# Kernel optimization log

Measured on AMD Instinct MI355X. Metric: run time of the kernel, lower is better.

## Reference

```python
import jax, jax.numpy as jnp
import numpy as np

B, N = 16, 512            # graphs, atoms per graph
F_DIM, H, D = 128, 64, 16  # feature_dim, hidden_dim, far_source_dim
CUT, GROWTH = 5.0, 2.0
NS, NT = 3, 2
MULT = GROWTH ** NS        # default far_max_radius_multiplier = 8
EMAX = CUT * MULT          # 40.0
TOT = NS + NT              # 5 shells total
SF = D + 3                 # 19 per-shell features
SE_IN = TOT * SF           # 95
EH_IN = 4 * D + SE_IN      # 159
N_RBF = 8
BOUNDS = [(5.0, 10.0), (10.0, 20.0), (20.0, 40.0), (40.0, 80.0), (80.0, float('inf'))]


def ln(x, g, b):
    m = x.mean(-1, keepdims=True)
    v = x.var(-1, keepdims=True)
    return (x - m) / jnp.sqrt(v + 1e-5) * g + b


def setup_inputs() -> dict:
    key = jax.random.key(0)
    ks = jax.random.split(key, 16)
    W = lambda k, i, o: jax.random.normal(k, (i, o), jnp.float32) / np.sqrt(i)
    inp = {}
    inp['x'] = jax.random.normal(ks[0], (B * N, F_DIM), jnp.float32)
    inp['pos'] = jax.random.uniform(ks[1], (B * N, 3), jnp.float32) * 80.0
    inp['batch'] = jnp.repeat(jnp.arange(B, dtype=jnp.int32), N)
    inp['num_graphs'] = B
    inp['in_ln_g'] = jnp.ones(F_DIM); inp['in_ln_b'] = jnp.zeros(F_DIM)
    inp['src_w1'] = W(ks[2], F_DIM, H); inp['src_b1'] = jnp.zeros(H)
    inp['src_w2'] = W(ks[3], H, D);     inp['src_b2'] = jnp.zeros(D)
    inp['src_ln_g'] = jnp.ones(D); inp['src_ln_b'] = jnp.zeros(D)
    inp['se_ln_g'] = jnp.ones(SE_IN); inp['se_ln_b'] = jnp.zeros(SE_IN)
    inp['se_w1'] = W(ks[4], SE_IN, H); inp['se_b1'] = jnp.zeros(H)
    inp['se_w2'] = W(ks[5], H, D);     inp['se_b2'] = jnp.zeros(D)
    inp['eh_ln_g'] = jnp.ones(EH_IN); inp['eh_ln_b'] = jnp.zeros(EH_IN)
    inp['eh_w1'] = W(ks[6], EH_IN, H); inp['eh_b1'] = jnp.zeros(H)
    inp['eh_w2'] = W(ks[7], H, 1);     inp['eh_b2'] = jnp.zeros(1)
    inp['k_screen'] = jnp.float32(-8.0)
    inp['kg_w1'] = W(ks[8], N_RBF + 2, 32); inp['kg_b1'] = jnp.zeros(32)
    inp['kg_w2'] = jnp.zeros((32, 1)); inp['kg_b2'] = jnp.zeros(1)  # zero-init per source
    inp['far_gate'] = jnp.float32(0.2)
    inp['energy_scale'] = jnp.float32(0.0)
    return inp


def reference(x, pos, batch, num_graphs, in_ln_g, in_ln_b, src_w1, src_b1, src_w2, src_b2,
              src_ln_g, src_ln_b, se_ln_g, se_ln_b, se_w1, se_b1, se_w2, se_b2,
              eh_ln_g, eh_ln_b, eh_w1, eh_b1, eh_w2, eh_b2,
              k_screen, kg_w1, kg_b1, kg_w2, kg_b2, far_gate, energy_scale):
    M = x.shape[0]
    n = M // num_graphs
    # per-atom source features
    h = ln(x, in_ln_g, in_ln_b)
    src = jax.nn.silu(h @ src_w1 + src_b1) @ src_w2 + src_b2
    src = ln(src, src_ln_g, src_ln_b)
    # graph-wise neutralization (subtract per-graph mean)
    gsum = jax.ops.segment_sum(src, batch, num_segments=num_graphs)
    cnt = jax.ops.segment_sum(jnp.ones((M, 1), x.dtype), batch, num_segments=num_graphs)
    src = src - (gsum / jnp.maximum(cnt, 1.0))[batch]
    # pairwise distances per graph
    p = pos.reshape(num_graphs, n, 3)
    s = src.reshape(num_graphs, n, D)
    diff = p[:, :, None, :] - p[:, None, :, :]
    d = jnp.sqrt((diff * diff).sum(-1) + 1e-12)  # [B,n,n]
    not_self = ~jnp.eye(n, dtype=bool)[None]
    # physical kernel with learned RBF gate
    screening = jax.nn.softplus(k_screen)
    base = jnp.exp(-screening * d) / jnp.maximum(d, 1e-6)
    centers = jnp.linspace(CUT, EMAX, N_RBF)
    spacing = (EMAX - CUT) / (N_RBF - 1)
    gamma = 1.0 / (spacing * spacing)
    dc = d[..., None]
    rbf = jnp.exp(-gamma * (dc - centers) ** 2)
    gin = jnp.concatenate([dc / CUT, dc / EMAX, rbf], -1)
    gate = 1.0 + jnp.tanh(jax.nn.silu(gin @ kg_w1 + kg_b1) @ kg_w2 + kg_b2)[..., 0]
    ker = base * gate
    # shell statistics: kernel-weighted mean source, count, mean_r, rms_r per shell
    feats = []
    for lo, up in BOUNDS:
        m = (d >= lo) & not_self
        if np.isfinite(up):
            m = m & (d < up)
        mf = m.astype(x.dtype)
        c = mf.sum(-1)
        denom = jnp.maximum(c, 1.0)
        mean = jnp.einsum('bij,bjc->bic', ker * mf, s) / denom[..., None]
        mr = (mf * d).sum(-1) / denom
        rr = jnp.sqrt((mf * d * d).sum(-1) / denom + 1e-12)
        feats.append(jnp.concatenate([mean, c[..., None], mr[..., None], rr[..., None]], -1))
    shell = jnp.concatenate(feats, -1).reshape(M, SE_IN)  # [M, 95]
    emb = jax.nn.silu(ln(shell, se_ln_g, se_ln_b) @ se_w1 + se_b1) @ se_w2 + se_b2
    ein = jnp.concatenate([src, emb, src * emb, src - emb, shell], -1)  # [M, 159]
    pa = (jax.nn.silu(ln(ein, eh_ln_g, eh_ln_b) @ eh_w1 + eh_b1) @ eh_w2 + eh_b2)[..., 0]
    pa = pa * jnp.tanh(far_gate) * jnp.exp(energy_scale)
    return jax.ops.segment_sum(pa, batch, num_segments=num_graphs)  # per-graph energies [B]
```

## Files before the change

### kernel.cpp

```cpp
#include <hip/hip_runtime.h>
#include <hip/hip_bf16.h>
#include <math.h>

#define B_G   16
#define N_A   512
#define M_AT  8192
#define FD    128
#define HD    64
#define DD    16
#define SEIN  95
#define EHIN  159
#define NLUT  512
#define DMAXF 140.0f

__device__ __forceinline__ float silu_f(float z) { return z / (1.f + __expf(-z)); }

__global__ __launch_bounds__(128) void k_front(
    const float* __restrict__ x,
    const float* __restrict__ g, const float* __restrict__ bb,
    const float* __restrict__ w1, const float* __restrict__ b1,
    const float* __restrict__ w2, const float* __restrict__ b2,
    const float* __restrict__ lng, const float* __restrict__ lnb,
    const float* __restrict__ k_screen,
    const float* __restrict__ kg_w1, const float* __restrict__ kg_b1,
    const float* __restrict__ kg_w2, const float* __restrict__ kg_b2,
    float* __restrict__ srcout, float* __restrict__ partials,
    float2* __restrict__ lut, float* __restrict__ out) {
  int t = threadIdx.x;

  if (blockIdx.x >= 256) {
    int lb = blockIdx.x - 256;
    __shared__ float w1l[320], b1l[32], w2l[32];
    if (lb == 0 && t < B_G) out[t] = 0.f;
    for (int idx = t; idx < 320; idx += 128) w1l[idx] = kg_w1[idx];
    if (t < 32) { b1l[t] = kg_b1[t]; w2l[t] = kg_w2[t]; }
    __syncthreads();
    int i = lb * 128 + t;
    float step = DMAXF / (float)(NLUT - 1);
    float ksv = k_screen[0];
    float screening = fmaxf(ksv, 0.f) + log1pf(expf(-fabsf(ksv)));
    float b2v = kg_b2[0];
    float vals[2];
#pragma unroll
    for (int e = 0; e < 2; ++e) {
      int ii = min(i + e, NLUT - 1);
      float d = (float)ii * step;
      float base = expf(-screening * d) / fmaxf(d, 1e-6f);
      float gin[10];
      gin[0] = d * (1.f / 5.0f);
      gin[1] = d * (1.f / 40.0f);
#pragma unroll
      for (int kk = 0; kk < 8; ++kk) {
        float u = d - (5.0f + 5.0f * (float)kk);
        gin[2 + kk] = expf(-(1.f / 25.f) * u * u);
      }
      float accv = 0.f;
      for (int h = 0; h < 32; ++h) {
        float z = b1l[h];
#pragma unroll
        for (int kk = 0; kk < 10; ++kk) z += gin[kk] * w1l[kk * 32 + h];
        accv += silu_f(z) * w2l[h];
      }
      vals[e] = base * (1.f + tanhf(accv + b2v));
    }
    lut[i] = make_float2(vals[0], vals[1] - vals[0]);
    return;
  }

  int wave = t >> 6, lane = t & 63;
  __shared__ __align__(16) float xnsA[2][FD][16];
  __shared__ __align__(16) float hbA[2][HD][16];
  __shared__ float psum[2][16];

  int aBase = blockIdx.x * 32 + wave * 16;
  int al = lane & 15, prt = lane >> 4;

  float xr[32];
  const float4* xp = (const float4*)(x + (size_t)(aBase + al) * FD + prt * 32);
#pragma unroll
  for (int i = 0; i < 8; ++i) {
    float4 v = xp[i];
    xr[i*4] = v.x; xr[i*4+1] = v.y; xr[i*4+2] = v.z; xr[i*4+3] = v.w;
  }
  float s = 0.f;
#pragma unroll
  for (int i = 0; i < 32; ++i) s += xr[i];
  s += __shfl_xor(s, 16); s += __shfl_xor(s, 32);
  float m = s * (1.f / 128.f);
  float v2 = 0.f;
#pragma unroll
  for (int i = 0; i < 32; ++i) { float d = xr[i] - m; v2 += d * d; }
  v2 += __shfl_xor(v2, 16); v2 += __shfl_xor(v2, 32);
  float inv = rsqrtf(v2 * (1.f / 128.f) + 1e-5f);
#pragma unroll
  for (int i = 0; i < 32; ++i) {
    int k = prt * 32 + i;
    xnsA[wave][k][al] = (xr[i] - m) * inv * g[k] + bb[k];
  }
  __syncthreads();

  int h0 = al * 4, a0 = prt * 4;
  float acc[4][4] = {};
#pragma unroll 4
  for (int k = 0; k < FD; ++k) {
    float4 wv = ((const float4*)(w1 + (size_t)k * HD))[al];
    float4 xa = *(const float4*)&xnsA[wave][k][a0];
    acc[0][0] += wv.x * xa.x; acc[0][1] += wv.x * xa.y; acc[0][2] += wv.x * xa.z; acc[0][3] += wv.x * xa.w;
    acc[1][0] += wv.y * xa.x; acc[1][1] += wv.y * xa.y; acc[1][2] += wv.y * xa.z; acc[1][3] += wv.y * xa.w;
    acc[2][0] += wv.z * xa.x; acc[2][1] += wv.z * xa.y; acc[2][2] += wv.z * xa.z; acc[2][3] += wv.z * xa.w;
    acc[3][0] += wv.w * xa.x; acc[3][1] += wv.w * xa.y; acc[3][2] += wv.w * xa.z; acc[3][3] += wv.w * xa.w;
  }
  {
    float4 bv = ((const float4*)b1)[al];
    float bh[4] = {bv.x, bv.y, bv.z, bv.w};
#pragma unroll
    for (int i = 0; i < 4; ++i) {
      float4 o;
      o.x = silu_f(acc[i][0] + bh[i]); o.y = silu_f(acc[i][1] + bh[i]);
      o.z = silu_f(acc[i][2] + bh[i]); o.w = silu_f(acc[i][3] + bh[i]);
      *(float4*)&hbA[wave][h0 + i][a0] = o;
    }
  }
  __syncthreads();

  float acc2[4] = {};
#pragma unroll 4
  for (int h = 0; h < HD; ++h) {
    float wv = w2[h * DD + al];
    float4 hv = *(const float4*)&hbA[wave][h][a0];
    acc2[0] += wv * hv.x; acc2[1] += wv * hv.y; acc2[2] += wv * hv.z; acc2[3] += wv * hv.w;
  }
  float b2c = b2[al], lgc = lng[al], lbc = lnb[al];
  float lsum = 0.f;
#pragma unroll
  for (int j = 0; j < 4; ++j) {
    float val = acc2[j] + b2c;
    float sm = val;
    sm += __shfl_xor(sm, 1); sm += __shfl_xor(sm, 2); sm += __shfl_xor(sm, 4); sm += __shfl_xor(sm, 8);
    float mm = sm * (1.f / 16.f);
    float dv = val - mm;
    float vv = dv * dv;
    vv += __shfl_xor(vv, 1); vv += __shfl_xor(vv, 2); vv += __shfl_xor(vv, 4); vv += __shfl_xor(vv, 8);
    float iv = rsqrtf(vv * (1.f / 16.f) + 1e-5f);
    float ov = dv * iv * lgc + lbc;
    srcout[(size_t)(aBase + a0 + j) * DD + al] = ov;
    lsum += ov;
  }
  lsum += __shfl_xor(lsum, 16); lsum += __shfl_xor(lsum, 32);
  if (lane < 16) psum[wave][al] = lsum;
  __syncthreads();
  if (t < 16) partials[(size_t)blockIdx.x * 16 + t] = psum[0][t] + psum[1][t];
}

__global__ __launch_bounds__(256) void k_pairs(
    const float* __restrict__ pos, const float* __restrict__ src,
    const float2* __restrict__ lut, const float* __restrict__ partials,
    float* __restrict__ shell) {
  int gph = blockIdx.x >> 7;
  int blk = blockIdx.x & 127;
  int t = threadIdx.x, wave = t >> 6, lane = t & 63;
  int i_local = blk * 4 + wave;

  __shared__ __align__(16) float sp[N_A * 3];
  __shared__ __align__(16) float ss[N_A * DD];
  __shared__ __align__(16) float2 luts[NLUT];
  __shared__ __align__(16) float wb[4][N_A];
  __shared__ unsigned char tbs[4][N_A];
  __shared__ float smean[16];

  for (int idx = t; idx < N_A * 3 / 4; idx += 256)
    ((float4*)sp)[idx] = ((const float4*)(pos + (size_t)gph * N_A * 3))[idx];
  for (int idx = t; idx < N_A * DD / 4; idx += 256)
    ((float4*)ss)[idx] = ((const float4*)(src + (size_t)gph * N_A * DD))[idx];
  if (t < NLUT / 2) ((float4*)luts)[t] = ((const float4*)lut)[t];
  if (t < 64) {
    int c = t & 15, grp = t >> 4;
    float sm = 0.f;
#pragma unroll
    for (int k = 0; k < 4; ++k)
      sm += partials[(size_t)(gph * 16 + grp * 4 + k) * 16 + c];
    sm += __shfl_xor(sm, 16); sm += __shfl_xor(sm, 32);
    if (t < 16) smean[c] = sm * (1.f / 512.f);
  }
  __syncthreads();

  float px = sp[i_local * 3], py = sp[i_local * 3 + 1], pz = sp[i_local * 3 + 2];
  float cnt[5] = {0,0,0,0,0}, sd[5] = {0,0,0,0,0}, sdd[5] = {0,0,0,0,0}, sw[5] = {0,0,0,0,0};
  const float lscale = (float)(NLUT - 1) / DMAXF;

#pragma unroll
  for (int it = 0; it < 8; ++it) {
    int jv = lane + it * 64;
    float dx = px - sp[jv * 3], dy = py - sp[jv * 3 + 1], dz = pz - sp[jv * 3 + 2];
    float d2 = dx * dx + dy * dy + dz * dz + 1e-12f;
    float d = sqrtf(d2);
    bool valid = (jv != i_local) && (d >= 5.0f);
    int tq = (d >= 10.f) + (d >= 20.f) + (d >= 40.f) + (d >= 80.f);
    float xq = d * lscale;
    int i0 = min((int)xq, NLUT - 2);
    float f = xq - (float)i0;
    float2 L = luts[i0];
    float w = valid ? (L.x + L.y * f) : 0.f;
    wb[wave][jv] = w;
    tbs[wave][jv] = (unsigned char)tq;
    float dm = valid ? d : 0.f;
    float ddm = valid ? d * d : 0.f;
    float cm = valid ? 1.f : 0.f;
#pragma unroll
    for (int q = 0; q < 5; ++q) {
      bool mq = (tq == q);
      cnt[q] += mq ? cm : 0.f;
      sd[q]  += mq ? dm : 0.f;
      sdd[q] += mq ? ddm : 0.f;
      sw[q]  += mq ? w : 0.f;
    }
  }
#pragma unroll
  for (int q = 0; q < 5; ++q) {
#pragma unroll
    for (int o = 32; o > 0; o >>= 1) {
      cnt[q] += __shfl_xor(cnt[q], o);
      sd[q]  += __shfl_xor(sd[q], o);
      sdd[q] += __shfl_xor(sdd[q], o);
      sw[q]  += __shfl_xor(sw[q], o);
    }
  }
  __syncthreads();

  int jlow = lane & 15, cq = lane >> 4;
  float accq[5][4] = {};
  const float* ssb = &ss[jlow * DD + cq * 4];
  const float* wbb = &wb[wave][jlow];
  const unsigned char* tbb = &tbs[wave][jlow];
#pragma unroll
  for (int jj = 0; jj < 32; ++jj) {
    float4 sv = *(const float4*)(ssb + jj * 256);
    float w = wbb[jj * 16];
    int tq = tbb[jj * 16];
    float w0 = (tq == 0) ? w : 0.f;
    float w1_ = (tq == 1) ? w : 0.f;
    float w2_ = (tq == 2) ? w : 0.f;
    float w3_ = (tq == 3) ? w : 0.f;
    float w4_ = (tq == 4) ? w : 0.f;
    accq[0][0] += w0 * sv.x; accq[0][1] += w0 * sv.y; accq[0][2] += w0 * sv.z; accq[0][3] += w0 * sv.w;
    accq[1][0] += w1_ * sv.x; accq[1][1] += w1_ * sv.y; accq[1][2] += w1_ * sv.z; accq[1][3] += w1_ * sv.w;
    accq[2][0] += w2_ * sv.x; accq[2][1] += w2_ * sv.y; accq[2][2] += w2_ * sv.z; accq[2][3] += w2_ * sv.w;
    accq[3][0] += w3_ * sv.x; accq[3][1] += w3_ * sv.y; accq[3][2] += w3_ * sv.z; accq[3][3] += w3_ * sv.w;
    accq[4][0] += w4_ * sv.x; accq[4][1] += w4_ * sv.y; accq[4][2] += w4_ * sv.z; accq[4][3] += w4_ * sv.w;
  }
#pragma unroll
  for (int q = 0; q < 5; ++q)
#pragma unroll
    for (int i = 0; i < 4; ++i) {
      float v = accq[q][i];
      v += __shfl_xor(v, 1); v += __shfl_xor(v, 2); v += __shfl_xor(v, 4); v += __shfl_xor(v, 8);
      accq[q][i] = v;
    }

  float* shp = shell + (size_t)(gph * N_A + i_local) * SEIN;
  if (jlow == 0) {
#pragma unroll
    for (int q = 0; q < 5; ++q) {
      float denom = fmaxf(cnt[q], 1.f);
#pragma unroll
      for (int i = 0; i < 4; ++i) {
        int c = cq * 4 + i;
        shp[q * 19 + c] = (accq[q][i] - smean[c] * sw[q]) / denom;
      }
    }
  }
  if (lane < 5) {
    int q = lane;
    float denom = fmaxf(cnt[q], 1.f);
    shp[q * 19 + 16] = cnt[q];
    shp[q * 19 + 17] = sd[q] / denom;
    shp[q * 19 + 18] = sqrtf(sdd[q] / denom + 1e-12f);
  }
}

__global__ __launch_bounds__(128) void k_tail(
    const float* __restrict__ src, const float* __restrict__ shell,
    const float* __restrict__ partials,
    const float* __restrict__ se_ln_g, const float* __restrict__ se_ln_b,
    const float* __restrict__ se_w1, const float* __restrict__ se_b1,
    const float* __restrict__ se_w2, const float* __restrict__ se_b2,
    const float* __restrict__ eh_ln_g, const float* __restrict__ eh_ln_b,
    const float* __restrict__ eh_w1, const float* __restrict__ eh_b1,
    const float* __restrict__ eh_w2, const float* __restrict__ eh_b2,
    const float* __restrict__ far_gate, const float* __restrict__ energy_scale,
    float* __restrict__ out) {
  int t = threadIdx.x, wave = t >> 6, lane = t & 63;
  __shared__ __align__(16) float einA[2][EHIN][16];
  __shared__ __align__(16) float shnA[2][SEIN][16];
  __shared__ __align__(16) float hbA[2][HD][16];
  __shared__ float smean[16];
  __shared__ float redv[2][4];

  int aB = blockIdx.x * 32;
  int gph = aB >> 9;

  if (t < 64) {
    int c = t & 15, grp = t >> 4;
    float sm = 0.f;
#pragma unroll
    for (int k = 0; k < 4; ++k)
      sm += partials[(size_t)(gph * 16 + grp * 4 + k) * 16 + c];
    sm += __shfl_xor(sm, 16); sm += __shfl_xor(sm, 32);
    if (t < 16) smean[c] = sm * (1.f / 512.f);
  }

  const float* shg = shell + (size_t)aB * SEIN;
  for (int idx = t; idx < 32 * SEIN; idx += 128) {
    unsigned a_loc = ((unsigned)idx * 690u) >> 16;
    int kk = idx - (int)a_loc * SEIN;
    einA[a_loc >> 4][64 + kk][a_loc & 15] = shg[idx];
  }
  __syncthreads();

  int al = lane & 15, prt = lane >> 4;
  {
    float s1 = 0.f, sq = 0.f;
    for (int i = 0; i < 24; ++i) {
      int k = prt * 24 + i;
      if (k < SEIN) { float v = einA[wave][64 + k][al]; s1 += v; sq += v * v; }
    }
    s1 += __shfl_xor(s1, 16); s1 += __shfl_xor(s1, 32);
    sq += __shfl_xor(sq, 16); sq += __shfl_xor(sq, 32);
    float m = s1 * (1.f / (float)SEIN);
    float var = sq * (1.f / (float)SEIN) - m * m;
    float inv = rsqrtf(var + 1e-5f);
    for (int i = 0; i < 24; ++i) {
      int k = prt * 24 + i;
      if (k < SEIN)
        shnA[wave][k][al] = (einA[wave][64 + k][al] - m) * inv * se_ln_g[k] + se_ln_b[k];
    }
  }
  __syncthreads();

  int h0 = al * 4, a0 = prt * 4;
  {
    float acc[4][4] = {};
#pragma unroll 5
    for (int k = 0; k < SEIN; ++k) {
      float4 wv = ((const float4*)(se_w1 + (size_t)k * HD))[al];
      float4 xa = *(const float4*)&shnA[wave][k][a0];
      acc[0][0] += wv.x * xa.x; acc[0][1] += wv.x * xa.y; acc[0][2] += wv.x * xa.z; acc[0][3] += wv.x * xa.w;
      acc[1][0] += wv.y * xa.x; acc[1][1] += wv.y * xa.y; acc[1][2] += wv.y * xa.z; acc[1][3] += wv.y * xa.w;
      acc[2][0] += wv.z * xa.x; acc[2][1] += wv.z * xa.y; acc[2][2] += wv.z * xa.z; acc[2][3] += wv.z * xa.w;
      acc[3][0] += wv.w * xa.x; acc[3][1] += wv.w * xa.y; acc[3][2] += wv.w * xa.z; acc[3][3] += wv.w * xa.w;
    }
    float4 bv = ((const float4*)se_b1)[al];
    float bh[4] = {bv.x, bv.y, bv.z, bv.w};
#pragma unroll
    for (int i = 0; i < 4; ++i) {
      float4 o;
      o.x = silu_f(acc[i][0] + bh[i]); o.y = silu_f(acc[i][1] + bh[i]);
      o.z = silu_f(acc[i][2] + bh[i]); o.w = silu_f(acc[i][3] + bh[i]);
      *(float4*)&hbA[wave][h0 + i][a0] = o;
    }
  }
  __syncthreads();

  {
    float acc2[4] = {};
#pragma unroll 4
    for (int h = 0; h < HD; ++h) {
      float wv = se_w2[h * DD + al];
      float4 hv = *(const float4*)&hbA[wave][h][a0];
      acc2[0] += wv * hv.x; acc2[1] += wv * hv.y; acc2[2] += wv * hv.z; acc2[3] += wv * hv.w;
    }
    float b2c = se_b2[al], smc = smean[al];
    int aW = aB + wave * 16;
#pragma unroll
    for (int j = 0; j < 4; ++j) {
      float ev = acc2[j] + b2c;
      float sv = src[(size_t)(aW + a0 + j) * DD + al] - smc;
      einA[wave][al][a0 + j] = sv;
      einA[wave][16 + al][a0 + j] = ev;
      einA[wave][32 + al][a0 + j] = sv * ev;
      einA[wave][48 + al][a0 + j] = sv - ev;
    }
  }
  __syncthreads();

  {
    float s1 = 0.f, sq = 0.f;
    for (int i = 0; i < 40; ++i) {
      int k = prt * 40 + i;
      if (k < EHIN) { float v = einA[wave][k][al]; s1 += v; sq += v * v; }
    }
    s1 += __shfl_xor(s1, 16); s1 += __shfl_xor(s1, 32);
    sq += __shfl_xor(sq, 16); sq += __shfl_xor(sq, 32);
    float m = s1 * (1.f / (float)EHIN);
    float var = sq * (1.f / (float)EHIN) - m * m;
    float inv = rsqrtf(var + 1e-5f);
    for (int i = 0; i < 40; ++i) {
      int k = prt * 40 + i;
      if (k < EHIN)
        einA[wave][k][al] = (einA[wave][k][al] - m) * inv * eh_ln_g[k] + eh_ln_b[k];
    }
  }
  __syncthreads();

  {
    float acc[4][4] = {};
#pragma unroll 3
    for (int k = 0; k < EHIN; ++k) {
      float4 wv = ((const float4*)(eh_w1 + (size_t)k * HD))[al];
      float4 xa = *(const float4*)&einA[wave][k][a0];
      acc[0][0] += wv.x * xa.x; acc[0][1] += wv.x * xa.y; acc[0][2] += wv.x * xa.z; acc[0][3] += wv.x * xa.w;
      acc[1][0] += wv.y * xa.x; acc[1][1] += wv.y * xa.y; acc[1][2] += wv.y * xa.z; acc[1][3] += wv.y * xa.w;
      acc[2][0] += wv.z * xa.x; acc[2][1] += wv.z * xa.y; acc[2][2] += wv.z * xa.z; acc[2][3] += wv.z * xa.w;
      acc[3][0] += wv.w * xa.x; acc[3][1] += wv.w * xa.y; acc[3][2] += wv.w * xa.z; acc[3][3] += wv.w * xa.w;
    }
    float4 b1v = ((const float4*)eh_b1)[al];
    float4 w2v = ((const float4*)eh_w2)[al];
    float bh[4] = {b1v.x, b1v.y, b1v.z, b1v.w};
    float wh[4] = {w2v.x, w2v.y, w2v.z, w2v.w};
    float pa[4] = {0.f, 0.f, 0.f, 0.f};
#pragma unroll
    for (int i = 0; i < 4; ++i)
#pragma unroll
      for (int j = 0; j < 4; ++j) pa[j] += silu_f(acc[i][j] + bh[i]) * wh[i];
#pragma unroll
    for (int j = 0; j < 4; ++j) {
      pa[j] += __shfl_xor(pa[j], 1); pa[j] += __shfl_xor(pa[j], 2);
      pa[j] += __shfl_xor(pa[j], 4); pa[j] += __shfl_xor(pa[j], 8);
    }
    if (al == 0) redv[wave][prt] = pa[0] + pa[1] + pa[2] + pa[3] + 4.f * eh_b2[0];
  }
  __syncthreads();
  if (t == 0) {
    float tot = 0.f;
#pragma unroll
    for (int w_ = 0; w_ < 2; ++w_)
#pragma unroll
      for (int p = 0; p < 4; ++p) tot += redv[w_][p];
    atomicAdd(&out[gph], tot * tanhf(far_gate[0]) * expf(energy_scale[0]));
  }
}

extern "C" void kernel_launch(void* const* d_in, const int* in_sizes, int n_in,
                              void* d_out, int out_size, void* d_ws, size_t ws_size,
                              hipStream_t stream) {
  const float* x         = (const float*)d_in[0];
  const float* pos       = (const float*)d_in[1];
  const float* in_ln_g   = (const float*)d_in[4];
  const float* in_ln_b   = (const float*)d_in[5];
  const float* src_w1    = (const float*)d_in[6];
  const float* src_b1    = (const float*)d_in[7];
  const float* src_w2    = (const float*)d_in[8];
  const float* src_b2    = (const float*)d_in[9];
  const float* src_ln_g  = (const float*)d_in[10];
  const float* src_ln_b  = (const float*)d_in[11];
  const float* se_ln_g   = (const float*)d_in[12];
  const float* se_ln_b   = (const float*)d_in[13];
  const float* se_w1     = (const float*)d_in[14];
  const float* se_b1     = (const float*)d_in[15];
  const float* se_w2     = (const float*)d_in[16];
  const float* se_b2     = (const float*)d_in[17];
  const float* eh_ln_g   = (const float*)d_in[18];
  const float* eh_ln_b   = (const float*)d_in[19];
  const float* eh_w1     = (const float*)d_in[20];
  const float* eh_b1     = (const float*)d_in[21];
  const float* eh_w2     = (const float*)d_in[22];
  const float* eh_b2     = (const float*)d_in[23];
  const float* k_screen  = (const float*)d_in[24];
  const float* kg_w1     = (const float*)d_in[25];
  const float* kg_b1     = (const float*)d_in[26];
  const float* kg_w2     = (const float*)d_in[27];
  const float* kg_b2     = (const float*)d_in[28];
  const float* far_gate  = (const float*)d_in[29];
  const float* en_scale  = (const float*)d_in[30];
  float* out = (float*)d_out;

  float* ws_src   = (float*)d_ws;
  float* ws_shell = ws_src + (size_t)M_AT * DD;
  float* ws_part  = ws_shell + (size_t)M_AT * SEIN;
  float2* ws_lut  = (float2*)(ws_part + 256 * 16);

  k_front<<<260, 128, 0, stream>>>(x, in_ln_g, in_ln_b, src_w1, src_b1,
                                   src_w2, src_b2, src_ln_g, src_ln_b,
                                   k_screen, kg_w1, kg_b1, kg_w2, kg_b2,
                                   ws_src, ws_part, ws_lut, out);
  k_pairs<<<B_G * (N_A / 4), 256, 0, stream>>>(pos, ws_src, ws_lut, ws_part, ws_shell);
  k_tail<<<M_AT / 32, 128, 0, stream>>>(ws_src, ws_shell, ws_part,
                                        se_ln_g, se_ln_b, se_w1, se_b1, se_w2, se_b2,
                                        eh_ln_g, eh_ln_b, eh_w1, eh_b1, eh_w2, eh_b2,
                                        far_gate, en_scale, out);
}
```

Baseline: 209.3 us.

## Fuse pair-shell and tail MLP kernels, restructure front MLP to 8 atoms per block

Merges the pairwise shell-statistics kernel with the tail MLP kernel so each wave computes its atom's shell features and runs the se/eh MLPs straight from shared memory, removing the global shell buffer round trip and one launch. The pair loop now fuses distance/LUT evaluation with the weighted source accumulation instead of staging weights and shell indices in shared memory. The front kernel is reshaped to 4 atoms per wave and 1024 blocks, so the partial-sum layout changes. The per-atom MLPs in the fused kernel run as GEMV with one atom per wave, which loses the weight reuse across atoms that the old register-tiled 4x4 scheme had, and some pair-loop work is now done redundantly by each 16-lane group.

```diff
diff --git a/kernel.cpp b/kernel.cpp
--- a/kernel.cpp
+++ b/kernel.cpp
@@ -28,9 +28,13 @@
     float2* __restrict__ lut, float* __restrict__ out) {
   int t = threadIdx.x;
 
-  if (blockIdx.x >= 256) {
-    int lb = blockIdx.x - 256;
-    __shared__ float w1l[320], b1l[32], w2l[32];
+  __shared__ __align__(16) float xns[2][FD][5];
+  __shared__ __align__(16) float hb[2][HD][5];
+  __shared__ float psum[2][16];
+  __shared__ float w1l[320], b1l[32], w2l[32];
+
+  if (blockIdx.x >= 1024) {
+    int lb = blockIdx.x - 1024;
     if (lb == 0 && t < B_G) out[t] = 0.f;
     for (int idx = t; idx < 320; idx += 128) w1l[idx] = kg_w1[idx];
     if (t < 32) { b1l[t] = kg_b1[t]; w2l[t] = kg_w2[t]; }
@@ -68,94 +72,86 @@
   }
 
   int wave = t >> 6, lane = t & 63;
-  __shared__ __align__(16) float xnsA[2][FD][16];
-  __shared__ __align__(16) float hbA[2][HD][16];
-  __shared__ float psum[2][16];
-
-  int aBase = blockIdx.x * 32 + wave * 16;
-  int al = lane & 15, prt = lane >> 4;
-
-  float xr[32];
-  const float4* xp = (const float4*)(x + (size_t)(aBase + al) * FD + prt * 32);
+  int a = lane >> 4;
+  int s = lane & 15;
+  int aBase = blockIdx.x * 8 + wave * 4;
+
+  float xr[8];
+  {
+    const float4* xp = (const float4*)(x + (size_t)(aBase + a) * FD + s * 8);
+    float4 v0 = xp[0], v1 = xp[1];
+    xr[0]=v0.x; xr[1]=v0.y; xr[2]=v0.z; xr[3]=v0.w;
+    xr[4]=v1.x; xr[5]=v1.y; xr[6]=v1.z; xr[7]=v1.w;
+  }
+  float sm_ = 0.f;
+#pragma unroll
+  for (int i = 0; i < 8; ++i) sm_ += xr[i];
+  sm_ += __shfl_xor(sm_, 1); sm_ += __shfl_xor(sm_, 2);
+  sm_ += __shfl_xor(sm_, 4); sm_ += __shfl_xor(sm_, 8);
+  float m = sm_ * (1.f / 128.f);
+  float v2 = 0.f;
+#pragma unroll
+  for (int i = 0; i < 8; ++i) { float d = xr[i] - m; v2 += d * d; }
+  v2 += __shfl_xor(v2, 1); v2 += __shfl_xor(v2, 2);
+  v2 += __shfl_xor(v2, 4); v2 += __shfl_xor(v2, 8);
+  float inv = rsqrtf(v2 * (1.f / 128.f) + 1e-5f);
 #pragma unroll
   for (int i = 0; i < 8; ++i) {
-    float4 v = xp[i];
-    xr[i*4] = v.x; xr[i*4+1] = v.y; xr[i*4+2] = v.z; xr[i*4+3] = v.w;
-  }
-  float s = 0.f;
-#pragma unroll
-  for (int i = 0; i < 32; ++i) s += xr[i];
-  s += __shfl_xor(s, 16); s += __shfl_xor(s, 32);
-  float m = s * (1.f / 128.f);
-  float v2 = 0.f;
-#pragma unroll
-  for (int i = 0; i < 32; ++i) { float d = xr[i] - m; v2 += d * d; }
-  v2 += __shfl_xor(v2, 16); v2 += __shfl_xor(v2, 32);
-  float inv = rsqrtf(v2 * (1.f / 128.f) + 1e-5f);
-#pragma unroll
-  for (int i = 0; i < 32; ++i) {
-    int k = prt * 32 + i;
-    xnsA[wave][k][al] = (xr[i] - m) * inv * g[k] + bb[k];
-  }
-  __syncthreads();
-
-  int h0 = al * 4, a0 = prt * 4;
-  float acc[4][4] = {};
-#pragma unroll 4
+    int k = s * 8 + i;
+    xns[wave][k][a] = (xr[i] - m) * inv * g[k] + bb[k];
+  }
+
+  float acc[4] = {0.f, 0.f, 0.f, 0.f};
+#pragma unroll 8
   for (int k = 0; k < FD; ++k) {
-    float4 wv = ((const float4*)(w1 + (size_t)k * HD))[al];
-    float4 xa = *(const float4*)&xnsA[wave][k][a0];
-    acc[0][0] += wv.x * xa.x; acc[0][1] += wv.x * xa.y; acc[0][2] += wv.x * xa.z; acc[0][3] += wv.x * xa.w;
-    acc[1][0] += wv.y * xa.x; acc[1][1] += wv.y * xa.y; acc[1][2] += wv.y * xa.z; acc[1][3] += wv.y * xa.w;
-    acc[2][0] += wv.z * xa.x; acc[2][1] += wv.z * xa.y; acc[2][2] += wv.z * xa.z; acc[2][3] += wv.z * xa.w;
-    acc[3][0] += wv.w * xa.x; acc[3][1] += wv.w * xa.y; acc[3][2] += wv.w * xa.z; acc[3][3] += wv.w * xa.w;
-  }
-  {
-    float4 bv = ((const float4*)b1)[al];
-    float bh[4] = {bv.x, bv.y, bv.z, bv.w};
-#pragma unroll
-    for (int i = 0; i < 4; ++i) {
-      float4 o;
-      o.x = silu_f(acc[i][0] + bh[i]); o.y = silu_f(acc[i][1] + bh[i]);
-      o.z = silu_f(acc[i][2] + bh[i]); o.w = silu_f(acc[i][3] + bh[i]);
-      *(float4*)&hbA[wave][h0 + i][a0] = o;
-    }
-  }
-  __syncthreads();
-
-  float acc2[4] = {};
-#pragma unroll 4
-  for (int h = 0; h < HD; ++h) {
-    float wv = w2[h * DD + al];
-    float4 hv = *(const float4*)&hbA[wave][h][a0];
-    acc2[0] += wv * hv.x; acc2[1] += wv * hv.y; acc2[2] += wv * hv.z; acc2[3] += wv * hv.w;
-  }
-  float b2c = b2[al], lgc = lng[al], lbc = lnb[al];
-  float lsum = 0.f;
-#pragma unroll
-  for (int j = 0; j < 4; ++j) {
-    float val = acc2[j] + b2c;
-    float sm = val;
-    sm += __shfl_xor(sm, 1); sm += __shfl_xor(sm, 2); sm += __shfl_xor(sm, 4); sm += __shfl_xor(sm, 8);
-    float mm = sm * (1.f / 16.f);
-    float dv = val - mm;
-    float vv = dv * dv;
-    vv += __shfl_xor(vv, 1); vv += __shfl_xor(vv, 2); vv += __shfl_xor(vv, 4); vv += __shfl_xor(vv, 8);
-    float iv = rsqrtf(vv * (1.f / 16.f) + 1e-5f);
-    float ov = dv * iv * lgc + lbc;
-    srcout[(size_t)(aBase + a0 + j) * DD + al] = ov;
-    lsum += ov;
-  }
+    float4 wv = ((const float4*)(w1 + (size_t)k * HD))[s];
+    float xa = xns[wave][k][a];
+    acc[0] += wv.x * xa; acc[1] += wv.y * xa;
+    acc[2] += wv.z * xa; acc[3] += wv.w * xa;
+  }
+  {
+    float4 bv = ((const float4*)b1)[s];
+    hb[wave][s * 4 + 0][a] = silu_f(acc[0] + bv.x);
+    hb[wave][s * 4 + 1][a] = silu_f(acc[1] + bv.y);
+    hb[wave][s * 4 + 2][a] = silu_f(acc[2] + bv.z);
+    hb[wave][s * 4 + 3][a] = silu_f(acc[3] + bv.w);
+  }
+
+  float e = 0.f;
+#pragma unroll 8
+  for (int k = 0; k < HD; ++k) e += hb[wave][k][a] * w2[k * DD + s];
+  float val = e + b2[s];
+
+  float smv = val;
+  smv += __shfl_xor(smv, 1); smv += __shfl_xor(smv, 2);
+  smv += __shfl_xor(smv, 4); smv += __shfl_xor(smv, 8);
+  float mm = smv * (1.f / 16.f);
+  float dv = val - mm;
+  float vv = dv * dv;
+  vv += __shfl_xor(vv, 1); vv += __shfl_xor(vv, 2);
+  vv += __shfl_xor(vv, 4); vv += __shfl_xor(vv, 8);
+  float iv = rsqrtf(vv * (1.f / 16.f) + 1e-5f);
+  float ov = dv * iv * lng[s] + lnb[s];
+  srcout[(size_t)(aBase + a) * DD + s] = ov;
+
+  float lsum = ov;
   lsum += __shfl_xor(lsum, 16); lsum += __shfl_xor(lsum, 32);
-  if (lane < 16) psum[wave][al] = lsum;
+  if (lane < 16) psum[wave][lane] = lsum;
   __syncthreads();
   if (t < 16) partials[(size_t)blockIdx.x * 16 + t] = psum[0][t] + psum[1][t];
 }
 
-__global__ __launch_bounds__(256) void k_pairs(
+__global__ __launch_bounds__(256) void k_pairs_tail(
     const float* __restrict__ pos, const float* __restrict__ src,
     const float2* __restrict__ lut, const float* __restrict__ partials,
-    float* __restrict__ shell) {
+    const float* __restrict__ se_ln_g, const float* __restrict__ se_ln_b,
+    const float* __restrict__ se_w1, const float* __restrict__ se_b1,
+    const float* __restrict__ se_w2, const float* __restrict__ se_b2,
+    const float* __restrict__ eh_ln_g, const float* __restrict__ eh_ln_b,
+    const float* __restrict__ eh_w1, const float* __restrict__ eh_b1,
+    const float* __restrict__ eh_w2, const float* __restrict__ eh_b2,
+    const float* __restrict__ far_gate, const float* __restrict__ energy_scale,
+    float* __restrict__ out) {
   int gph = blockIdx.x >> 7;
   int blk = blockIdx.x & 127;
   int t = threadIdx.x, wave = t >> 6, lane = t & 63;
@@ -164,9 +160,11 @@
   __shared__ __align__(16) float sp[N_A * 3];
   __shared__ __align__(16) float ss[N_A * DD];
   __shared__ __align__(16) float2 luts[NLUT];
-  __shared__ __align__(16) float wb[4][N_A];
-  __shared__ unsigned char tbs[4][N_A];
   __shared__ float smean[16];
+  __shared__ __align__(16) float einL[4][160];
+  __shared__ __align__(16) float shnL[4][96];
+  __shared__ __align__(16) float hbL[4][64];
+  __shared__ float redv[4];
 
   for (int idx = t; idx < N_A * 3 / 4; idx += 256)
     ((float4*)sp)[idx] = ((const float4*)(pos + (size_t)gph * N_A * 3))[idx];
@@ -177,87 +175,69 @@
     int c = t & 15, grp = t >> 4;
     float sm = 0.f;
 #pragma unroll
-    for (int k = 0; k < 4; ++k)
-      sm += partials[(size_t)(gph * 16 + grp * 4 + k) * 16 + c];
+    for (int kk = 0; kk < 16; ++kk)
+      sm += partials[(size_t)(gph * 64 + grp * 16 + kk) * 16 + c];
     sm += __shfl_xor(sm, 16); sm += __shfl_xor(sm, 32);
     if (t < 16) smean[c] = sm * (1.f / 512.f);
   }
   __syncthreads();
 
+  int jlow = lane & 15, cq = lane >> 4;
   float px = sp[i_local * 3], py = sp[i_local * 3 + 1], pz = sp[i_local * 3 + 2];
-  float cnt[5] = {0,0,0,0,0}, sd[5] = {0,0,0,0,0}, sdd[5] = {0,0,0,0,0}, sw[5] = {0,0,0,0,0};
+  float accq[5][4] = {};
+  float cnt[5] = {0,0,0,0,0}, sdv[5] = {0,0,0,0,0}, sdd[5] = {0,0,0,0,0}, swq[5] = {0,0,0,0,0};
   const float lscale = (float)(NLUT - 1) / DMAXF;
 
-#pragma unroll
-  for (int it = 0; it < 8; ++it) {
-    int jv = lane + it * 64;
-    float dx = px - sp[jv * 3], dy = py - sp[jv * 3 + 1], dz = pz - sp[jv * 3 + 2];
+#pragma unroll 8
+  for (int jj = 0; jj < 32; ++jj) {
+    int j = jj * 16 + jlow;
+    float dx = px - sp[j * 3], dy = py - sp[j * 3 + 1], dz = pz - sp[j * 3 + 2];
     float d2 = dx * dx + dy * dy + dz * dz + 1e-12f;
     float d = sqrtf(d2);
-    bool valid = (jv != i_local) && (d >= 5.0f);
+    bool valid = (j != i_local) && (d >= 5.0f);
     int tq = (d >= 10.f) + (d >= 20.f) + (d >= 40.f) + (d >= 80.f);
     float xq = d * lscale;
     int i0 = min((int)xq, NLUT - 2);
     float f = xq - (float)i0;
     float2 L = luts[i0];
     float w = valid ? (L.x + L.y * f) : 0.f;
-    wb[wave][jv] = w;
-    tbs[wave][jv] = (unsigned char)tq;
     float dm = valid ? d : 0.f;
     float ddm = valid ? d * d : 0.f;
     float cm = valid ? 1.f : 0.f;
+    float4 sv = *(const float4*)&ss[j * DD + cq * 4];
 #pragma unroll
     for (int q = 0; q < 5; ++q) {
       bool mq = (tq == q);
+      float wq = mq ? w : 0.f;
+      accq[q][0] += wq * sv.x; accq[q][1] += wq * sv.y;
+      accq[q][2] += wq * sv.z; accq[q][3] += wq * sv.w;
       cnt[q] += mq ? cm : 0.f;
-      sd[q]  += mq ? dm : 0.f;
+      sdv[q] += mq ? dm : 0.f;
       sdd[q] += mq ? ddm : 0.f;
-      sw[q]  += mq ? w : 0.f;
-    }
-  }
+      swq[q] += wq;
+    }
+  }
+#pragma unroll
+  for (int q = 0; q < 5; ++q)
+#pragma unroll
+    for (int i = 0; i < 4; ++i) {
+      float v = accq[q][i];
+      v += __shfl_xor(v, 1); v += __shfl_xor(v, 2);
+      v += __shfl_xor(v, 4); v += __shfl_xor(v, 8);
+      accq[q][i] = v;
+    }
 #pragma unroll
   for (int q = 0; q < 5; ++q) {
 #pragma unroll
     for (int o = 32; o > 0; o >>= 1) {
       cnt[q] += __shfl_xor(cnt[q], o);
-      sd[q]  += __shfl_xor(sd[q], o);
+      sdv[q] += __shfl_xor(sdv[q], o);
       sdd[q] += __shfl_xor(sdd[q], o);
-      sw[q]  += __shfl_xor(sw[q], o);
-    }
-  }
-  __syncthreads();
-
-  int jlow = lane & 15, cq = lane >> 4;
-  float accq[5][4] = {};
-  const float* ssb = &ss[jlow * DD + cq * 4];
-  const float* wbb = &wb[wave][jlow];
-  const unsigned char* tbb = &tbs[wave][jlow];
-#pragma unroll
-  for (int jj = 0; jj < 32; ++jj) {
-    float4 sv = *(const float4*)(ssb + jj * 256);
-    float w = wbb[jj * 16];
-    int tq = tbb[jj * 16];
-    float w0 = (tq == 0) ? w : 0.f;
-    float w1_ = (tq == 1) ? w : 0.f;
-    float w2_ = (tq == 2) ? w : 0.f;
-    float w3_ = (tq == 3) ? w : 0.f;
-    float w4_ = (tq == 4) ? w : 0.f;
-    accq[0][0] += w0 * sv.x; accq[0][1] += w0 * sv.y; accq[0][2] += w0 * sv.z; accq[0][3] += w0 * sv.w;
-    accq[1][0] += w1_ * sv.x; accq[1][1] += w1_ * sv.y; accq[1][2] += w1_ * sv.z; accq[1][3] += w1_ * sv.w;
-    accq[2][0] += w2_ * sv.x; accq[2][1] += w2_ * sv.y; accq[2][2] += w2_ * sv.z; accq[2][3] += w2_ * sv.w;
-    accq[3][0] += w3_ * sv.x; accq[3][1] += w3_ * sv.y; accq[3][2] += w3_ * sv.z; accq[3][3] += w3_ * sv.w;
-    accq[4][0] += w4_ * sv.x; accq[4][1] += w4_ * sv.y; accq[4][2] += w4_ * sv.z; accq[4][3] += w4_ * sv.w;
-  }
-#pragma unroll
-  for (int q = 0; q < 5; ++q)
-#pragma unroll
-    for (int i = 0; i < 4; ++i) {
-      float v = accq[q][i];
-      v += __shfl_xor(v, 1); v += __shfl_xor(v, 2); v += __shfl_xor(v, 4); v += __shfl_xor(v, 8);
-      accq[q][i] = v;
-    }
-
-  float* shp = shell + (size_t)(gph * N_A + i_local) * SEIN;
+      swq[q] += __shfl_xor(swq[q], o);
+    }
+    cnt[q] *= 0.25f; sdv[q] *= 0.25f; sdd[q] *= 0.25f; swq[q] *= 0.25f;
+  }
+
   if (jlow == 0) {
 #pragma unroll
     for (int q = 0; q < 5; ++q) {
@@ -265,177 +245,87 @@
 #pragma unroll
       for (int i = 0; i < 4; ++i) {
         int c = cq * 4 + i;
-        shp[q * 19 + c] = (accq[q][i] - smean[c] * sw[q]) / denom;
+        einL[wave][64 + q * 19 + c] = (accq[q][i] - smean[c] * swq[q]) / denom;
       }
     }
   }
   if (lane < 5) {
     int q = lane;
     float denom = fmaxf(cnt[q], 1.f);
-    shp[q * 19 + 16] = cnt[q];
-    shp[q * 19 + 17] = sd[q] / denom;
-    shp[q * 19 + 18] = sqrtf(sdd[q] / denom + 1e-12f);
-  }
-}
-
-__global__ __launch_bounds__(128) void k_tail(
-    const float* __restrict__ src, const float* __restrict__ shell,
-    const float* __restrict__ partials,
-    const float* __restrict__ se_ln_g, const float* __restrict__ se_ln_b,
-    const float* __restrict__ se_w1, const float* __restrict__ se_b1,
-    const float* __restrict__ se_w2, const float* __restrict__ se_b2,
-    const float* __restrict__ eh_ln_g, const float* __restrict__ eh_ln_b,
-    const float* __restrict__ eh_w1, const float* __restrict__ eh_b1,
-    const float* __restrict__ eh_w2, const float* __restrict__ eh_b2,
-    const float* __restrict__ far_gate, const float* __restrict__ energy_scale,
-    float* __restrict__ out) {
-  int t = threadIdx.x, wave = t >> 6, lane = t & 63;
-  __shared__ __align__(16) float einA[2][EHIN][16];
-  __shared__ __align__(16) float shnA[2][SEIN][16];
-  __shared__ __align__(16) float hbA[2][HD][16];
-  __shared__ float smean[16];
-  __shared__ float redv[2][4];
-
-  int aB = blockIdx.x * 32;
-  int gph = aB >> 9;
-
-  if (t < 64) {
-    int c = t & 15, grp = t >> 4;
-    float sm = 0.f;
-#pragma unroll
-    for (int k = 0; k < 4; ++k)
-      sm += partials[(size_t)(gph * 16 + grp * 4 + k) * 16 + c];
-    sm += __shfl_xor(sm, 16); sm += __shfl_xor(sm, 32);
-    if (t < 16) smean[c] = sm * (1.f / 512.f);
-  }
-
-  const float* shg = shell + (size_t)aB * SEIN;
-  for (int idx = t; idx < 32 * SEIN; idx += 128) {
-    unsigned a_loc = ((unsigned)idx * 690u) >> 16;
-    int kk = idx - (int)a_loc * SEIN;
-    einA[a_loc >> 4][64 + kk][a_loc & 15] = shg[idx];
-  }
-  __syncthreads();
-
-  int al = lane & 15, prt = lane >> 4;
-  {
-    float s1 = 0.f, sq = 0.f;
-    for (int i = 0; i < 24; ++i) {
-      int k = prt * 24 + i;
-      if (k < SEIN) { float v = einA[wave][64 + k][al]; s1 += v; sq += v * v; }
-    }
-    s1 += __shfl_xor(s1, 16); s1 += __shfl_xor(s1, 32);
-    sq += __shfl_xor(sq, 16); sq += __shfl_xor(sq, 32);
-    float m = s1 * (1.f / (float)SEIN);
-    float var = sq * (1.f / (float)SEIN) - m * m;
-    float inv = rsqrtf(var + 1e-5f);
-    for (int i = 0; i < 24; ++i) {
-      int k = prt * 24 + i;
-      if (k < SEIN)
-        shnA[wave][k][al] = (einA[wave][64 + k][al] - m) * inv * se_ln_g[k] + se_ln_b[k];
-    }
-  }
-  __syncthreads();
-
-  int h0 = al * 4, a0 = prt * 4;
-  {
-    float acc[4][4] = {};
+    einL[wave][64 + q * 19 + 16] = cnt[q];
+    einL[wave][64 + q * 19 + 17] = sdv[q] / denom;
+    einL[wave][64 + q * 19 + 18] = sqrtf(sdd[q] / denom + 1e-12f);
+  }
+
+  {
+    float v0 = einL[wave][64 + lane];
+    float v1 = (lane < 31) ? einL[wave][128 + lane] : 0.f;
+    float s1 = v0 + v1, sq = v0 * v0 + v1 * v1;
+#pragma unroll
+    for (int o = 32; o > 0; o >>= 1) { s1 += __shfl_xor(s1, o); sq += __shfl_xor(sq, o); }
+    float mn = s1 * (1.f / (float)SEIN);
+    float var = sq * (1.f / (float)SEIN) - mn * mn;
+    float invv = rsqrtf(var + 1e-5f);
+    shnL[wave][lane] = (v0 - mn) * invv * se_ln_g[lane] + se_ln_b[lane];
+    if (lane < 31)
+      shnL[wave][64 + lane] = (v1 - mn) * invv * se_ln_g[64 + lane] + se_ln_b[64 + lane];
+  }
+
+  {
+    float z = se_b1[lane];
 #pragma unroll 5
-    for (int k = 0; k < SEIN; ++k) {
-      float4 wv = ((const float4*)(se_w1 + (size_t)k * HD))[al];
-      float4 xa = *(const float4*)&shnA[wave][k][a0];
-      acc[0][0] += wv.x * xa.x; acc[0][1] += wv.x * xa.y; acc[0][2] += wv.x * xa.z; acc[0][3] += wv.x * xa.w;
-      acc[1][0] += wv.y * xa.x; acc[1][1] += wv.y * xa.y; acc[1][2] += wv.y * xa.z; acc[1][3] += wv.y * xa.w;
-      acc[2][0] += wv.z * xa.x; acc[2][1] += wv.z * xa.y; acc[2][2] += wv.z * xa.z; acc[2][3] += wv.z * xa.w;
-      acc[3][0] += wv.w * xa.x; acc[3][1] += wv.w * xa.y; acc[3][2] += wv.w * xa.z; acc[3][3] += wv.w * xa.w;
-    }
-    float4 bv = ((const float4*)se_b1)[al];
-    float bh[4] = {bv.x, bv.y, bv.z, bv.w};
-#pragma unroll
-    for (int i = 0; i < 4; ++i) {
-      float4 o;
-      o.x = silu_f(acc[i][0] + bh[i]); o.y = silu_f(acc[i][1] + bh[i]);
-      o.z = silu_f(acc[i][2] + bh[i]); o.w = silu_f(acc[i][3] + bh[i]);
-      *(float4*)&hbA[wave][h0 + i][a0] = o;
-    }
-  }
-  __syncthreads();
-
-  {
-    float acc2[4] = {};
-#pragma unroll 4
-    for (int h = 0; h < HD; ++h) {
-      float wv = se_w2[h * DD + al];
-      float4 hv = *(const float4*)&hbA[wave][h][a0];
-      acc2[0] += wv * hv.x; acc2[1] += wv * hv.y; acc2[2] += wv * hv.z; acc2[3] += wv * hv.w;
-    }
-    float b2c = se_b2[al], smc = smean[al];
-    int aW = aB + wave * 16;
-#pragma unroll
-    for (int j = 0; j < 4; ++j) {
-      float ev = acc2[j] + b2c;
-      float sv = src[(size_t)(aW + a0 + j) * DD + al] - smc;
-      einA[wave][al][a0 + j] = sv;
-      einA[wave][16 + al][a0 + j] = ev;
-      einA[wave][32 + al][a0 + j] = sv * ev;
-      einA[wave][48 + al][a0 + j] = sv - ev;
-    }
-  }
-  __syncthreads();
-
-  {
-    float s1 = 0.f, sq = 0.f;
-    for (int i = 0; i < 40; ++i) {
-      int k = prt * 40 + i;
-      if (k < EHIN) { float v = einA[wave][k][al]; s1 += v; sq += v * v; }
-    }
-    s1 += __shfl_xor(s1, 16); s1 += __shfl_xor(s1, 32);
-    sq += __shfl_xor(sq, 16); sq += __shfl_xor(sq, 32);
-    float m = s1 * (1.f / (float)EHIN);
-    float var = sq * (1.f / (float)EHIN) - m * m;
-    float inv = rsqrtf(var + 1e-5f);
-    for (int i = 0; i < 40; ++i) {
-      int k = prt * 40 + i;
-      if (k < EHIN)
-        einA[wave][k][al] = (einA[wave][k][al] - m) * inv * eh_ln_g[k] + eh_ln_b[k];
-    }
-  }
-  __syncthreads();
-
-  {
-    float acc[4][4] = {};
+    for (int k = 0; k < SEIN; ++k) z += shnL[wave][k] * se_w1[(size_t)k * HD + lane];
+    hbL[wave][lane] = silu_f(z);
+  }
+
+  {
+    int c = lane & 15, kq = lane >> 4;
+    float e = 0.f;
+#pragma unroll
+    for (int i = 0; i < 16; ++i) {
+      int k = kq * 16 + i;
+      e += hbL[wave][k] * se_w2[k * DD + c];
+    }
+    e += __shfl_down(e, 32);
+    e += __shfl_down(e, 16);
+    if (lane < 16) {
+      float ev = e + se_b2[lane];
+      float svv = ss[i_local * DD + lane] - smean[lane];
+      einL[wave][lane] = svv;
+      einL[wave][16 + lane] = ev;
+      einL[wave][32 + lane] = svv * ev;
+      einL[wave][48 + lane] = svv - ev;
+    }
+  }
+
+  {
+    float u0 = einL[wave][lane];
+    float u1 = einL[wave][64 + lane];
+    float u2 = (lane < 31) ? einL[wave][128 + lane] : 0.f;
+    float s1 = u0 + u1 + u2, sq = u0 * u0 + u1 * u1 + u2 * u2;
+#pragma unroll
+    for (int o = 32; o > 0; o >>= 1) { s1 += __shfl_xor(s1, o); sq += __shfl_xor(sq, o); }
+    float mn = s1 * (1.f / (float)EHIN);
+    float var = sq * (1.f / (float)EHIN) - mn * mn;
+    float invv = rsqrtf(var + 1e-5f);
+    einL[wave][lane] = (u0 - mn) * invv * eh_ln_g[lane] + eh_ln_b[lane];
+    einL[wave][64 + lane] = (u1 - mn) * invv * eh_ln_g[64 + lane] + eh_ln_b[64 + lane];
+    if (lane < 31)
+      einL[wave][128 + lane] = (u2 - mn) * invv * eh_ln_g[128 + lane] + eh_ln_b[128 + lane];
+  }
+
+  {
+    float z2 = eh_b1[lane];
 #pragma unroll 3
-    for (int k = 0; k < EHIN; ++k) {
-      float4 wv = ((const float4*)(eh_w1 + (size_t)k * HD))[al];
-      float4 xa = *(const float4*)&einA[wave][k][a0];
-      acc[0][0] += wv.x * xa.x; acc[0][1] += wv.x * xa.y; acc[0][2] += wv.x * xa.z; acc[0][3] += wv.x * xa.w;
-      acc[1][0] += wv.y * xa.x; acc[1][1] += wv.y * xa.y; acc[1][2] += wv.y * xa.z; acc[1][3] += wv.y * xa.w;
-      acc[2][0] += wv.z * xa.x; acc[2][1] += wv.z * xa.y; acc[2][2] += wv.z * xa.z; acc[2][3] += wv.z * xa.w;
-      acc[3][0] += wv.w * xa.x; acc[3][1] += wv.w * xa.y; acc[3][2] += wv.w * xa.z; acc[3][3] += wv.w * xa.w;
-    }
-    float4 b1v = ((const float4*)eh_b1)[al];
-    float4 w2v = ((const float4*)eh_w2)[al];
-    float bh[4] = {b1v.x, b1v.y, b1v.z, b1v.w};
-    float wh[4] = {w2v.x, w2v.y, w2v.z, w2v.w};
-    float pa[4] = {0.f, 0.f, 0.f, 0.f};
-#pragma unroll
-    for (int i = 0; i < 4; ++i)
-#pragma unroll
-      for (int j = 0; j < 4; ++j) pa[j] += silu_f(acc[i][j] + bh[i]) * wh[i];
-#pragma unroll
-    for (int j = 0; j < 4; ++j) {
-      pa[j] += __shfl_xor(pa[j], 1); pa[j] += __shfl_xor(pa[j], 2);
-      pa[j] += __shfl_xor(pa[j], 4); pa[j] += __shfl_xor(pa[j], 8);
-    }
-    if (al == 0) redv[wave][prt] = pa[0] + pa[1] + pa[2] + pa[3] + 4.f * eh_b2[0];
+    for (int k = 0; k < EHIN; ++k) z2 += einL[wave][k] * eh_w1[(size_t)k * HD + lane];
+    float pa = silu_f(z2) * eh_w2[lane];
+#pragma unroll
+    for (int o = 32; o > 0; o >>= 1) pa += __shfl_xor(pa, o);
+    if (lane == 0) redv[wave] = pa + eh_b2[0];
   }
   __syncthreads();
   if (t == 0) {
-    float tot = 0.f;
-#pragma unroll
-    for (int w_ = 0; w_ < 2; ++w_)
-#pragma unroll
-      for (int p = 0; p < 4; ++p) tot += redv[w_][p];
+    float tot = redv[0] + redv[1] + redv[2] + redv[3];
     atomicAdd(&out[gph], tot * tanhf(far_gate[0]) * expf(energy_scale[0]));
   }
 }
@@ -475,17 +365,16 @@
   float* out = (float*)d_out;
 
   float* ws_src   = (float*)d_ws;
-  float* ws_shell = ws_src + (size_t)M_AT * DD;
-  float* ws_part  = ws_shell + (size_t)M_AT * SEIN;
-  float2* ws_lut  = (float2*)(ws_part + 256 * 16);
-
-  k_front<<<260, 128, 0, stream>>>(x, in_ln_g, in_ln_b, src_w1, src_b1,
-                                   src_w2, src_b2, src_ln_g, src_ln_b,
-                                   k_screen, kg_w1, kg_b1, kg_w2, kg_b2,
-                                   ws_src, ws_part, ws_lut, out);
-  k_pairs<<<B_G * (N_A / 4), 256, 0, stream>>>(pos, ws_src, ws_lut, ws_part, ws_shell);
-  k_tail<<<M_AT / 32, 128, 0, stream>>>(ws_src, ws_shell, ws_part,
-                                        se_ln_g, se_ln_b, se_w1, se_b1, se_w2, se_b2,
-                                        eh_ln_g, eh_ln_b, eh_w1, eh_b1, eh_w2, eh_b2,
-                                        far_gate, en_scale, out);
+  float* ws_part  = ws_src + (size_t)M_AT * DD;
+  float2* ws_lut  = (float2*)(ws_part + 1024 * 16);
+
+  k_front<<<1028, 128, 0, stream>>>(x, in_ln_g, in_ln_b, src_w1, src_b1,
+                                    src_w2, src_b2, src_ln_g, src_ln_b,
+                                    k_screen, kg_w1, kg_b1, kg_w2, kg_b2,
+                                    ws_src, ws_part, ws_lut, out);
+  k_pairs_tail<<<B_G * (N_A / 4), 256, 0, stream>>>(
+      pos, ws_src, ws_lut, ws_part,
+      se_ln_g, se_ln_b, se_w1, se_b1, se_w2, se_b2,
+      eh_ln_g, eh_ln_b, eh_w1, eh_b1, eh_w2, eh_b2,
+      far_gate, en_scale, out);
 }
```

New measurement: 218.0 us. 1.04x slower.
